# Optimization experiments

Hardware: AMD Instinct MI355X
Metric: run time of the kernel (lower is better)

Reference implementation:

```python
import jax, jax.numpy as jnp
import numpy as np

N, D, R, E = 20000, 256, 12, 200000  # nodes, feat dim, relation labels, edges


def setup_inputs() -> dict:
    key = jax.random.key(0)
    ks = jax.random.split(key, 8)
    x = jax.random.normal(ks[0], (N, D), dtype=jnp.float32)
    dep_idx = jax.random.randint(ks[1], (E,), 0, N)
    rel_idx = jax.random.randint(ks[2], (E,), 0, R)
    gov_idx = jax.random.randint(ks[3], (E,), 0, N)
    # nn.Linear params: W is [out,in], y = x @ W.T + b
    W_self = jax.random.normal(ks[4], (D, D), dtype=jnp.float32) * 0.02
    b_self = jnp.zeros((D,), dtype=jnp.float32)
    # 2R relation weights: [0..R) forward labels, [R..2R) reversed '_r' labels
    W_rel = jax.random.normal(ks[5], (2 * R, D, D), dtype=jnp.float32) * 0.02
    b_rel = jax.random.normal(ks[6], (2 * R, D), dtype=jnp.float32) * 0.02
    return {"x": x, "dep_idx": dep_idx, "rel_idx": rel_idx, "gov_idx": gov_idx,
            "W_self": W_self, "b_self": b_self, "W_rel": W_rel, "b_rel": b_rel}


def reference(x, dep_idx, rel_idx, gov_idx, W_self, b_self, W_rel, b_rel):
    R_ = W_rel.shape[0] // 2
    # self transform for every node
    out = x @ W_self.T + b_self  # [N, D]
    # all-relation transform, grouped GEMM instead of per-edge Linear calls
    T = jnp.einsum('nd,rod->nro', x, W_rel)  # [N, 2R, D]
    # forward edges: dependent += W[rel] @ x[governor] + b[rel]
    msg_f = T[gov_idx, rel_idx] + b_rel[rel_idx]          # [E, D]
    # reverse edges: governor += W[rel_r] @ x[dependent] + b[rel_r]
    msg_r = T[dep_idx, rel_idx + R_] + b_rel[rel_idx + R_]  # [E, D]
    out = out.at[dep_idx].add(msg_f).at[gov_idx].add(msg_r)
    return jax.nn.relu(out)
```

## Files before the change

### kernel.cpp

```cpp
#include <hip/hip_runtime.h>
#include <cstdint>
#include <cstddef>

#define DD 256
#define NSLOT 25
#define SELFSLOT 12

typedef unsigned short u16;
typedef __bf16 bf16t;
typedef bf16t bf16x8 __attribute__((ext_vector_type(8)));
typedef unsigned short us8 __attribute__((ext_vector_type(8)));
typedef unsigned short us4 __attribute__((ext_vector_type(4)));
typedef float f32x4 __attribute__((ext_vector_type(4)));

__device__ __forceinline__ u16 f2bf(float f) {
    uint32_t u = __builtin_bit_cast(uint32_t, f);
    u += 0x7FFFu + ((u >> 16) & 1u);
    return (u16)(u >> 16);
}
__device__ __forceinline__ float bf2f(u16 h) {
    uint32_t u = ((uint32_t)h) << 16;
    return __builtin_bit_cast(float, u);
}

__global__ void k_prep(const float* __restrict__ x, const float* __restrict__ W_rel,
                       const float* __restrict__ W_self, const float* __restrict__ b_self,
                       const float* __restrict__ b_rel,
                       u16* __restrict__ xb, u16* __restrict__ Wb, float* __restrict__ ba,
                       const int* __restrict__ dep, const int* __restrict__ rel,
                       const int* __restrict__ gov, int E, int N, int SG,
                       int* __restrict__ flag, int* __restrict__ bcnt, int NDD) {
    if (blockIdx.x < 1024) {
        const int s0 = NDD;
        const int s1 = s0 + 12 * 65536;
        const int s2 = s1 + 65536;
        const int s3 = s2 + 12 * 65536;
        const int s4 = s3 + NSLOT * DD;
        int i = blockIdx.x * 256 + threadIdx.x;
        int st = 1024 * 256;
        for (; i < s4; i += st) {
            if (i < s0) {
                xb[i] = f2bf(x[i]);
            } else if (i < s1) {
                int k = i - s0; Wb[k] = f2bf(W_rel[k]);
            } else if (i < s2) {
                int k = i - s1; Wb[12 * 65536 + k] = f2bf(W_self[k]);
            } else if (i < s3) {
                int k = i - s2; Wb[13 * 65536 + k] = f2bf(W_rel[12 * 65536 + k]);
            } else {
                int k = i - s3;
                float v;
                if (k < 12 * DD) v = b_rel[k];
                else if (k < 13 * DD) v = b_self[k - 12 * DD];
                else v = b_rel[k - DD];
                ba[k] = v;
            }
        }
    } else {
        int i = (blockIdx.x - 1024) * 256 + threadIdx.x;
        int st = 512 * 256;
        for (int j = i; j < E; j += st) {
            int r = rel[j], d = dep[j], g = gov[j];
            flag[r * N + g] = 1;
            flag[(13 + r) * N + d] = 1;
            atomicAdd(&bcnt[(r / SG) * N + d], 1);
            atomicAdd(&bcnt[((13 + r) / SG) * N + g], 1);
        }
        for (int j = i; j < N; j += st) flag[SELFSLOT * N + j] = 1;
    }
}

__global__ void k_scan1d(const int* __restrict__ A, int* __restrict__ outA,
                         int* __restrict__ bsumA, int lenA, int nbA,
                         const int* __restrict__ B, int* __restrict__ outB,
                         int* __restrict__ bsumB, int lenB) {
    __shared__ int sm[256];
    const int* in; int* outp; int* bs; int len; int lb;
    if ((int)blockIdx.x < nbA) { in = A; outp = outA; bs = bsumA; len = lenA; lb = blockIdx.x; }
    else { in = B; outp = outB; bs = bsumB; len = lenB; lb = blockIdx.x - nbA; }
    int tid = threadIdx.x;
    int i = lb * 256 + tid;
    int v = (i < len) ? in[i] : 0;
    sm[tid] = v;
    __syncthreads();
    for (int off = 1; off < 256; off <<= 1) {
        int t = (tid >= off) ? sm[tid - off] : 0;
        __syncthreads();
        sm[tid] += t;
        __syncthreads();
    }
    if (i < len) outp[i] = sm[tid] - v;
    if (tid == 255) bs[lb] = sm[255];
}

__global__ void k_scan2d(const int* __restrict__ bsumA, int* __restrict__ bbasA, int nbA,
                         const int* __restrict__ bsumB, int* __restrict__ bbasB, int nbB) {
    __shared__ int sm[256];
    int t = threadIdx.x;
    for (int which = 0; which < 2; ++which) {
        const int* bsum = which ? bsumB : bsumA;
        int* bbase = which ? bbasB : bbasA;
        int nb = which ? nbB : nbA;
        int pre[8];
        int tot = 0;
        for (int j = 0; j < 8; ++j) {
            int idx = t * 8 + j;
            int v = (idx < nb) ? bsum[idx] : 0;
            pre[j] = tot;
            tot += v;
        }
        sm[t] = tot;
        __syncthreads();
        for (int off = 1; off < 256; off <<= 1) {
            int x = (t >= off) ? sm[t - off] : 0;
            __syncthreads();
            sm[t] += x;
            __syncthreads();
        }
        int base = sm[t] - tot;
        for (int j = 0; j < 8; ++j) {
            int idx = t * 8 + j;
            if (idx < nb) bbase[idx] = base + pre[j];
        }
        __syncthreads();
    }
}

__global__ void k_scan3d(int* __restrict__ pos, const int* __restrict__ bbasA,
                         const int* __restrict__ flag, int NN, int N,
                         int* __restrict__ rksrc,
                         int* __restrict__ bcsr, int* __restrict__ bcur,
                         const int* __restrict__ bbasB, int B2, int E2) {
    int i = blockIdx.x * 256 + threadIdx.x;
    if (i < NN) {
        int v = pos[i] + bbasA[i >> 8];
        pos[i] = v;
        if (i == NN - 1) pos[NN] = v + flag[i];
        if (flag[i]) {
            int slot = i / N;
            rksrc[v] = i - slot * N;
        }
    }
    if (i < B2) {
        int v = bcsr[i] + bbasB[i >> 8];
        bcsr[i] = v;
        bcur[i] = v;
    }
    if (i == 0) bcsr[B2] = E2;
}

__global__ __launch_bounds__(256, 4) void k_T(
    const u16* __restrict__ xb, const u16* __restrict__ Wb, const float* __restrict__ ba,
    const int* __restrict__ pos, const int* __restrict__ rksrc, u16* __restrict__ T,
    int N, int gslot0, int Sg,
    const int* __restrict__ dep, const int* __restrict__ rel, const int* __restrict__ gov,
    int E, int SG, int* __restrict__ bcur, int* __restrict__ epay, int nScat) {
    __shared__ u16 sm[2 * 128 * 72];
    __shared__ int s_src[128];
    u16 (*As)[72] = (u16(*)[72])sm;
    u16 (*Bs)[72] = (u16(*)[72])(sm + 128 * 72);

    const int tid = threadIdx.x;
    if ((int)blockIdx.x < nScat) {
        int i = blockIdx.x * 256 + tid;
        int st = nScat * 256;
        for (; i < E; i += st) {
            int r = rel[i], d = dep[i], g = gov[i];
            int g0 = r / SG;
            int p = atomicAdd(&bcur[g0 * N + d], 1);
            epay[p] = pos[r * N + g] - pos[g0 * SG * N];
            int gs = 13 + r;
            int g1 = gs / SG;
            int q = atomicAdd(&bcur[g1 * N + g], 1);
            epay[q] = pos[gs * N + d] - pos[g1 * SG * N];
        }
        return;
    }

    const int bx = blockIdx.x - nScat;
    const int mtile = bx / (2 * Sg);
    const int rem = bx - mtile * 2 * Sg;
    const int slot = rem >> 1;
    const int n0 = (rem & 1) * 128;
    const int gslot = gslot0 + slot;
    const int u0 = pos[gslot * N];
    const int used = pos[(gslot + 1) * N] - u0;
    const int row0 = mtile * 128;
    if (row0 >= used) return;
    const int gbase = pos[gslot0 * N];

    if (tid < 128) {
        int r = row0 + tid;
        s_src[tid] = rksrc[u0 + ((r < used) ? r : (used - 1))];
    }
    __syncthreads();

    const int lane = tid & 63, wv = tid >> 6;
    const int wr = wv & 1, wc = wv >> 1;
    const int l15 = lane & 15, quad = lane >> 4;
    const int srow = tid >> 1, sh = (tid & 1) * 32;
    const u16* bgp = Wb + ((size_t)gslot << 16) + (size_t)(n0 + srow) * DD + sh;

    f32x4 acc[4][4] = {};
    for (int kb = 0; kb < DD; kb += 64) {
        {
            const us8* ga = (const us8*)(xb + (size_t)s_src[srow] * DD + kb + sh);
            us8 a0 = ga[0], a1 = ga[1], a2 = ga[2], a3 = ga[3];
            *(us8*)&As[srow][sh]      = a0;
            *(us8*)&As[srow][sh + 8]  = a1;
            *(us8*)&As[srow][sh + 16] = a2;
            *(us8*)&As[srow][sh + 24] = a3;
            const us8* gb = (const us8*)(bgp + kb);
            us8 b0 = gb[0], b1 = gb[1], b2 = gb[2], b3 = gb[3];
            *(us8*)&Bs[srow][sh]      = b0;
            *(us8*)&Bs[srow][sh + 8]  = b1;
            *(us8*)&Bs[srow][sh + 16] = b2;
            *(us8*)&Bs[srow][sh + 24] = b3;
        }
        __syncthreads();
        #pragma unroll
        for (int ks = 0; ks < 2; ++ks) {
            const int kk = ks * 32 + quad * 8;
            bf16x8 af[4], bfv[4];
            #pragma unroll
            for (int mt = 0; mt < 4; ++mt)
                af[mt] = __builtin_bit_cast(bf16x8, *(const us8*)&As[wr * 64 + mt * 16 + l15][kk]);
            #pragma unroll
            for (int nt = 0; nt < 4; ++nt)
                bfv[nt] = __builtin_bit_cast(bf16x8, *(const us8*)&Bs[wc * 64 + nt * 16 + l15][kk]);
            #pragma unroll
            for (int nt = 0; nt < 4; ++nt)
                #pragma unroll
                for (int mt = 0; mt < 4; ++mt)
                    acc[nt][mt] = __builtin_amdgcn_mfma_f32_16x16x32_bf16(
                        bfv[nt], af[mt], acc[nt][mt], 0, 0, 0);
        }
        __syncthreads();
    }

    f32x4 bb[4];
    #pragma unroll
    for (int nt = 0; nt < 4; ++nt)
        bb[nt] = *(const f32x4*)(ba + gslot * DD + n0 + wc * 64 + nt * 16 + quad * 4);
    u16* trb = sm + wv * (64 * 72);
    #pragma unroll
    for (int mt = 0; mt < 4; ++mt)
        #pragma unroll
        for (int nt = 0; nt < 4; ++nt) {
            us4 t4;
            #pragma unroll
            for (int j = 0; j < 4; ++j) t4[j] = f2bf(acc[nt][mt][j] + bb[nt][j]);
            *(us4*)&trb[(size_t)(mt * 16 + l15) * 72 + nt * 16 + quad * 4] = t4;
        }
    __syncthreads();
    const int trow0 = u0 - gbase + row0 + wr * 64;
    const int half = lane & 1;
    #pragma unroll
    for (int it = 0; it < 2; ++it) {
        int r = it * 32 + (lane >> 1);
        if (row0 + wr * 64 + r < used) {
            const us8* sp = (const us8*)(trb + r * 72 + half * 32);
            us8 v0 = sp[0], v1 = sp[1], v2 = sp[2], v3 = sp[3];
            us8* dp = (us8*)(T + (size_t)(trow0 + r) * DD + n0 + wc * 64 + half * 32);
            dp[0] = v0; dp[1] = v1; dp[2] = v2; dp[3] = v3;
        }
    }
}

__global__ __launch_bounds__(256) void k_gather(
    const u16* __restrict__ T, const int* __restrict__ epay,
    const int* __restrict__ csr, const int* __restrict__ pos,
    float* __restrict__ out, int N, int bktBase, int selfKeyBase, int gfN,
    int first, int last) {
    int wid = (blockIdx.x * 256 + threadIdx.x) >> 6;
    if (wid >= N) return;
    int feat = (threadIdx.x & 63) * 4;
    f32x4 a = {0.0f, 0.0f, 0.0f, 0.0f};
    if (!first) a = *(const f32x4*)(out + (size_t)wid * DD + feat);
    if (selfKeyBase >= 0) {
        int p = pos[selfKeyBase + wid] - pos[gfN];
        us4 v = *(const us4*)(T + (size_t)p * DD + feat);
        a[0] += bf2f(v[0]); a[1] += bf2f(v[1]); a[2] += bf2f(v[2]); a[3] += bf2f(v[3]);
    }
    int beg = csr[bktBase + wid], end = csr[bktBase + wid + 1];
    f32x4 b = {0, 0, 0, 0}, c = {0, 0, 0, 0}, d4 = {0, 0, 0, 0};
    int j = beg;
    for (; j + 7 < end; j += 8) {
        int p0 = epay[j],     p1 = epay[j + 1], p2 = epay[j + 2], p3 = epay[j + 3];
        int p4 = epay[j + 4], p5 = epay[j + 5], p6 = epay[j + 6], p7 = epay[j + 7];
        us4 v0 = *(const us4*)(T + (size_t)p0 * DD + feat);
        us4 v1 = *(const us4*)(T + (size_t)p1 * DD + feat);
        us4 v2 = *(const us4*)(T + (size_t)p2 * DD + feat);
        us4 v3 = *(const us4*)(T + (size_t)p3 * DD + feat);
        us4 v4 = *(const us4*)(T + (size_t)p4 * DD + feat);
        us4 v5 = *(const us4*)(T + (size_t)p5 * DD + feat);
        us4 v6 = *(const us4*)(T + (size_t)p6 * DD + feat);
        us4 v7 = *(const us4*)(T + (size_t)p7 * DD + feat);
        #pragma unroll
        for (int t = 0; t < 4; ++t) {
            a[t]  += bf2f(v0[t]) + bf2f(v4[t]);
            b[t]  += bf2f(v1[t]) + bf2f(v5[t]);
            c[t]  += bf2f(v2[t]) + bf2f(v6[t]);
            d4[t] += bf2f(v3[t]) + bf2f(v7[t]);
        }
    }
    for (; j + 1 < end; j += 2) {
        int p0 = epay[j], p1 = epay[j + 1];
        us4 v0 = *(const us4*)(T + (size_t)p0 * DD + feat);
        us4 v1 = *(const us4*)(T + (size_t)p1 * DD + feat);
        #pragma unroll
        for (int t = 0; t < 4; ++t) { a[t] += bf2f(v0[t]); b[t] += bf2f(v1[t]); }
    }
    if (j < end) {
        int p0 = epay[j];
        us4 v0 = *(const us4*)(T + (size_t)p0 * DD + feat);
        #pragma unroll
        for (int t = 0; t < 4; ++t) a[t] += bf2f(v0[t]);
    }
    #pragma unroll
    for (int t = 0; t < 4; ++t) a[t] += b[t] + c[t] + d4[t];
    if (last) {
        #pragma unroll
        for (int t = 0; t < 4; ++t) a[t] = fmaxf(a[t], 0.0f);
    }
    *(f32x4*)(out + (size_t)wid * DD + feat) = a;
}

extern "C" void kernel_launch(void* const* d_in, const int* in_sizes, int n_in,
                              void* d_out, int out_size, void* d_ws, size_t ws_size,
                              hipStream_t stream) {
    const float* x      = (const float*)d_in[0];
    const int*   dep    = (const int*)  d_in[1];
    const int*   rel    = (const int*)  d_in[2];
    const int*   gov    = (const int*)  d_in[3];
    const float* W_self = (const float*)d_in[4];
    const float* b_self = (const float*)d_in[5];
    const float* W_rel  = (const float*)d_in[6];
    const float* b_rel  = (const float*)d_in[7];
    float* out = (float*)d_out;

    const int N  = in_sizes[0] / DD;
    const int E  = in_sizes[1];
    const int NN = NSLOT * N;

    char* w = (char*)d_ws;
    auto alloc = [&](size_t bytes) {
        char* p = w;
        w += (bytes + 255) & ~(size_t)255;
        return p;
    };
    u16* xb    = (u16*)alloc((size_t)N * DD * sizeof(u16));
    u16* Wb    = (u16*)alloc((size_t)NSLOT * DD * DD * sizeof(u16));
    float* ba  = (float*)alloc((size_t)NSLOT * DD * sizeof(float));
    int* flag  = (int*)alloc((size_t)NN * sizeof(int));
    int* pos   = (int*)alloc(((size_t)NN + 1) * sizeof(int));
    int* rksrc = (int*)alloc(((size_t)2 * E + N) * sizeof(int));
    int* bcnt  = (int*)alloc((size_t)6 * N * sizeof(int));
    int* bcsr  = (int*)alloc(((size_t)6 * N + 1) * sizeof(int));
    int* bcur  = (int*)alloc((size_t)6 * N * sizeof(int));
    int* bsumA = (int*)alloc((size_t)2048 * sizeof(int));
    int* bbasA = (int*)alloc((size_t)2048 * sizeof(int));
    int* bsumB = (int*)alloc((size_t)2048 * sizeof(int));
    int* bbasB = (int*)alloc((size_t)2048 * sizeof(int));
    int* epay  = (int*)alloc((size_t)2 * E * sizeof(int));

    size_t used = (size_t)(w - (char*)d_ws);
    size_t avail = (ws_size > used) ? (ws_size - used) : 0;

    int NGROUP = 2, SG = 13;
    for (int ng = 1; ng <= 5; ++ng) {
        int sg = (NSLOT + ng - 1) / ng;
        size_t maxB = 0;
        for (int g = 0; g < ng; ++g) {
            int s0 = g * sg, s1 = s0 + sg; if (s1 > NSLOT) s1 = NSLOT;
            if (s0 >= NSLOT) break;
            int hasSelf = (s0 <= SELFSLOT && SELFSLOT < s1) ? 1 : 0;
            size_t rels = (size_t)(s1 - s0 - hasSelf);
            size_t rows = rels * N; if (rows > (size_t)2 * E) rows = (size_t)2 * E;
            rows += hasSelf ? (size_t)N : 0;
            if (rows > maxB) maxB = rows;
        }
        if (maxB * ((size_t)DD * 2) <= avail) { NGROUP = ng; SG = sg; break; }
        NGROUP = ng + 1; SG = (NSLOT + NGROUP - 1) / NGROUP;
    }
    u16* T = (u16*)w;
    const int B2 = NGROUP * N;

    hipMemsetAsync(flag, 0, (size_t)NN * sizeof(int), stream);
    hipMemsetAsync(bcnt, 0, (size_t)B2 * sizeof(int), stream);
    k_prep<<<1536, 256, 0, stream>>>(x, W_rel, W_self, b_self, b_rel, xb, Wb, ba,
                                     dep, rel, gov, E, N, SG, flag, bcnt, N * DD);

    const int nbA = (NN + 255) / 256;
    const int nbB = (B2 + 255) / 256;
    k_scan1d<<<nbA + nbB, 256, 0, stream>>>(flag, pos, bsumA, NN, nbA, bcnt, bcsr, bsumB, B2);
    k_scan2d<<<1, 256, 0, stream>>>(bsumA, bbasA, nbA, bsumB, bbasB, nbB);
    k_scan3d<<<nbA, 256, 0, stream>>>(pos, bbasA, flag, NN, N, rksrc, bcsr, bcur, bbasB, B2, 2 * E);

    const int tilesPerSlot = (N + 127) / 128;
    const int gBlocks = (N + 3) / 4;
    for (int g = 0; g < NGROUP; ++g) {
        int s0 = g * SG;
        if (s0 >= NSLOT) break;
        int Sg = NSLOT - s0; if (Sg > SG) Sg = SG;
        int nScat = (g == 0) ? 256 : 0;
        k_T<<<dim3(nScat + tilesPerSlot * Sg * 2), 256, 0, stream>>>(
            xb, Wb, ba, pos, rksrc, T, N, s0, Sg,
            dep, rel, gov, E, SG, bcur, epay, nScat);
        int hasSelf = (s0 <= SELFSLOT && SELFSLOT < s0 + Sg);
        k_gather<<<gBlocks, 256, 0, stream>>>(
            T, epay, bcsr, pos, out, N, g * N,
            hasSelf ? SELFSLOT * N : -1, s0 * N,
            (g == 0) ? 1 : 0, (g == NGROUP - 1) ? 1 : 0);
    }
}
```

Baseline: 260.7 us.

## Replace flag prefix scan with atomic per-slot compaction for unique rows

```diff
diff --git a/kernel.cpp b/kernel.cpp
--- a/kernel.cpp
+++ b/kernel.cpp
@@ -29,7 +29,9 @@
                        u16* __restrict__ xb, u16* __restrict__ Wb, float* __restrict__ ba,
                        const int* __restrict__ dep, const int* __restrict__ rel,
                        const int* __restrict__ gov, int E, int N, int SG,
-                       int* __restrict__ flag, int* __restrict__ bcnt, int NDD) {
+                       int* __restrict__ flag, int* __restrict__ slotcnt,
+                       int* __restrict__ bcnt, int* __restrict__ pos,
+                       int* __restrict__ rkpad, int NDD) {
     if (blockIdx.x < 1024) {
         const int s0 = NDD;
         const int s1 = s0 + 12 * 65536;
@@ -57,30 +59,53 @@
             }
         }
     } else {
+        __shared__ int lcnt[NSLOT], lbase[NSLOT];
+        if (threadIdx.x < NSLOT) lcnt[threadIdx.x] = 0;
+        __syncthreads();
         int i = (blockIdx.x - 1024) * 256 + threadIdx.x;
         int st = 512 * 256;
+        int wslot[4], wloc[4], wkey[4], wsrc[4];
+        int nw = 0;
         for (int j = i; j < E; j += st) {
             int r = rel[j], d = dep[j], g = gov[j];
-            flag[r * N + g] = 1;
-            flag[(13 + r) * N + d] = 1;
             atomicAdd(&bcnt[(r / SG) * N + d], 1);
             atomicAdd(&bcnt[((13 + r) / SG) * N + g], 1);
-        }
-        for (int j = i; j < N; j += st) flag[SELFSLOT * N + j] = 1;
-    }
-}
-
-__global__ void k_scan1d(const int* __restrict__ A, int* __restrict__ outA,
-                         int* __restrict__ bsumA, int lenA, int nbA,
-                         const int* __restrict__ B, int* __restrict__ outB,
-                         int* __restrict__ bsumB, int lenB) {
+            int kf = r * N + g;
+            if (atomicCAS(&flag[kf], 0, 1) == 0) {
+                wslot[nw] = r; wkey[nw] = kf; wsrc[nw] = g;
+                wloc[nw] = atomicAdd(&lcnt[r], 1);
+                ++nw;
+            }
+            int sr = 13 + r;
+            int kr = sr * N + d;
+            if (atomicCAS(&flag[kr], 0, 1) == 0) {
+                wslot[nw] = sr; wkey[nw] = kr; wsrc[nw] = d;
+                wloc[nw] = atomicAdd(&lcnt[sr], 1);
+                ++nw;
+            }
+        }
+        for (int j = i; j < N; j += st) {
+            pos[SELFSLOT * N + j] = j;
+            rkpad[SELFSLOT * N + j] = j;
+        }
+        __syncthreads();
+        if (threadIdx.x < NSLOT && lcnt[threadIdx.x] > 0)
+            lbase[threadIdx.x] = atomicAdd(&slotcnt[threadIdx.x], lcnt[threadIdx.x]);
+        __syncthreads();
+        for (int wv = 0; wv < nw; ++wv) {
+            int g = lbase[wslot[wv]] + wloc[wv];
+            pos[wkey[wv]] = g;
+            rkpad[wslot[wv] * N + g] = wsrc[wv];
+        }
+    }
+}
+
+__global__ void k_scan1(const int* __restrict__ B, int* __restrict__ outB,
+                        int* __restrict__ bsumB, int lenB) {
     __shared__ int sm[256];
-    const int* in; int* outp; int* bs; int len; int lb;
-    if ((int)blockIdx.x < nbA) { in = A; outp = outA; bs = bsumA; len = lenA; lb = blockIdx.x; }
-    else { in = B; outp = outB; bs = bsumB; len = lenB; lb = blockIdx.x - nbA; }
     int tid = threadIdx.x;
-    int i = lb * 256 + tid;
-    int v = (i < len) ? in[i] : 0;
+    int i = blockIdx.x * 256 + tid;
+    int v = (i < lenB) ? B[i] : 0;
     sm[tid] = v;
     __syncthreads();
     for (int off = 1; off < 256; off <<= 1) {
@@ -89,58 +114,48 @@
         sm[tid] += t;
         __syncthreads();
     }
-    if (i < len) outp[i] = sm[tid] - v;
-    if (tid == 255) bs[lb] = sm[255];
-}
-
-__global__ void k_scan2d(const int* __restrict__ bsumA, int* __restrict__ bbasA, int nbA,
-                         const int* __restrict__ bsumB, int* __restrict__ bbasB, int nbB) {
+    if (i < lenB) outB[i] = sm[tid] - v;
+    if (tid == 255) bsumB[blockIdx.x] = sm[255];
+}
+
+__global__ void k_scan2(const int* __restrict__ slotcnt, int* __restrict__ slotbase, int N,
+                        const int* __restrict__ bsumB, int* __restrict__ bbasB, int nbB) {
     __shared__ int sm[256];
     int t = threadIdx.x;
-    for (int which = 0; which < 2; ++which) {
-        const int* bsum = which ? bsumB : bsumA;
-        int* bbase = which ? bbasB : bbasA;
-        int nb = which ? nbB : nbA;
-        int pre[8];
-        int tot = 0;
-        for (int j = 0; j < 8; ++j) {
-            int idx = t * 8 + j;
-            int v = (idx < nb) ? bsum[idx] : 0;
-            pre[j] = tot;
-            tot += v;
-        }
-        sm[t] = tot;
-        __syncthreads();
-        for (int off = 1; off < 256; off <<= 1) {
-            int x = (t >= off) ? sm[t - off] : 0;
-            __syncthreads();
-            sm[t] += x;
-            __syncthreads();
-        }
-        int base = sm[t] - tot;
-        for (int j = 0; j < 8; ++j) {
-            int idx = t * 8 + j;
-            if (idx < nb) bbase[idx] = base + pre[j];
-        }
-        __syncthreads();
-    }
-}
-
-__global__ void k_scan3d(int* __restrict__ pos, const int* __restrict__ bbasA,
-                         const int* __restrict__ flag, int NN, int N,
-                         int* __restrict__ rksrc,
-                         int* __restrict__ bcsr, int* __restrict__ bcur,
-                         const int* __restrict__ bbasB, int B2, int E2) {
+    if (t == 0) {
+        int s = 0;
+        for (int k = 0; k < NSLOT; ++k) {
+            slotbase[k] = s;
+            s += (k == SELFSLOT) ? N : slotcnt[k];
+        }
+        slotbase[NSLOT] = s;
+    }
+    int pre[8];
+    int tot = 0;
+    for (int j = 0; j < 8; ++j) {
+        int idx = t * 8 + j;
+        int v = (idx < nbB) ? bsumB[idx] : 0;
+        pre[j] = tot;
+        tot += v;
+    }
+    sm[t] = tot;
+    __syncthreads();
+    for (int off = 1; off < 256; off <<= 1) {
+        int x = (t >= off) ? sm[t - off] : 0;
+        __syncthreads();
+        sm[t] += x;
+        __syncthreads();
+    }
+    int base = sm[t] - tot;
+    for (int j = 0; j < 8; ++j) {
+        int idx = t * 8 + j;
+        if (idx < nbB) bbasB[idx] = base + pre[j];
+    }
+}
+
+__global__ void k_scan3(int* __restrict__ bcsr, int* __restrict__ bcur,
+                        const int* __restrict__ bbasB, int B2, int E2) {
     int i = blockIdx.x * 256 + threadIdx.x;
-    if (i < NN) {
-        int v = pos[i] + bbasA[i >> 8];
-        pos[i] = v;
-        if (i == NN - 1) pos[NN] = v + flag[i];
-        if (flag[i]) {
-            int slot = i / N;
-            rksrc[v] = i - slot * N;
-        }
-    }
     if (i < B2) {
         int v = bcsr[i] + bbasB[i >> 8];
         bcsr[i] = v;
@@ -151,7 +166,8 @@
 
 __global__ __launch_bounds__(256, 4) void k_T(
     const u16* __restrict__ xb, const u16* __restrict__ Wb, const float* __restrict__ ba,
-    const int* __restrict__ pos, const int* __restrict__ rksrc, u16* __restrict__ T,
+    const int* __restrict__ slotbase, const int* __restrict__ pos,
+    const int* __restrict__ rkpad, u16* __restrict__ T,
     int N, int gslot0, int Sg,
     const int* __restrict__ dep, const int* __restrict__ rel, const int* __restrict__ gov,
     int E, int SG, int* __restrict__ bcur, int* __restrict__ epay, int nScat) {
@@ -168,11 +184,11 @@
             int r = rel[i], d = dep[i], g = gov[i];
             int g0 = r / SG;
             int p = atomicAdd(&bcur[g0 * N + d], 1);
-            epay[p] = pos[r * N + g] - pos[g0 * SG * N];
+            epay[p] = slotbase[r] + pos[r * N + g] - slotbase[g0 * SG];
             int gs = 13 + r;
             int g1 = gs / SG;
             int q = atomicAdd(&bcur[g1 * N + g], 1);
-            epay[q] = pos[gs * N + d] - pos[g1 * SG * N];
+            epay[q] = slotbase[gs] + pos[gs * N + d] - slotbase[g1 * SG];
         }
         return;
     }
@@ -183,15 +199,15 @@
     const int slot = rem >> 1;
     const int n0 = (rem & 1) * 128;
     const int gslot = gslot0 + slot;
-    const int u0 = pos[gslot * N];
-    const int used = pos[(gslot + 1) * N] - u0;
+    const int u0 = slotbase[gslot];
+    const int used = slotbase[gslot + 1] - u0;
     const int row0 = mtile * 128;
     if (row0 >= used) return;
-    const int gbase = pos[gslot0 * N];
+    const int gbase = slotbase[gslot0];
 
     if (tid < 128) {
         int r = row0 + tid;
-        s_src[tid] = rksrc[u0 + ((r < used) ? r : (used - 1))];
+        s_src[tid] = rkpad[gslot * N + ((r < used) ? r : (used - 1))];
     }
     __syncthreads();
 
@@ -269,16 +285,16 @@
 
 __global__ __launch_bounds__(256) void k_gather(
     const u16* __restrict__ T, const int* __restrict__ epay,
-    const int* __restrict__ csr, const int* __restrict__ pos,
-    float* __restrict__ out, int N, int bktBase, int selfKeyBase, int gfN,
+    const int* __restrict__ csr, const int* __restrict__ slotbase,
+    float* __restrict__ out, int N, int bktBase, int hasSelf, int s0,
     int first, int last) {
     int wid = (blockIdx.x * 256 + threadIdx.x) >> 6;
     if (wid >= N) return;
     int feat = (threadIdx.x & 63) * 4;
     f32x4 a = {0.0f, 0.0f, 0.0f, 0.0f};
     if (!first) a = *(const f32x4*)(out + (size_t)wid * DD + feat);
-    if (selfKeyBase >= 0) {
-        int p = pos[selfKeyBase + wid] - pos[gfN];
+    if (hasSelf) {
+        int p = slotbase[SELFSLOT] - slotbase[s0] + wid;
         us4 v = *(const us4*)(T + (size_t)p * DD + feat);
         a[0] += bf2f(v[0]); a[1] += bf2f(v[1]); a[2] += bf2f(v[2]); a[3] += bf2f(v[3]);
     }
@@ -352,17 +368,18 @@
     u16* xb    = (u16*)alloc((size_t)N * DD * sizeof(u16));
     u16* Wb    = (u16*)alloc((size_t)NSLOT * DD * DD * sizeof(u16));
     float* ba  = (float*)alloc((size_t)NSLOT * DD * sizeof(float));
-    int* flag  = (int*)alloc((size_t)NN * sizeof(int));
-    int* pos   = (int*)alloc(((size_t)NN + 1) * sizeof(int));
-    int* rksrc = (int*)alloc(((size_t)2 * E + N) * sizeof(int));
-    int* bcnt  = (int*)alloc((size_t)6 * N * sizeof(int));
-    int* bcsr  = (int*)alloc(((size_t)6 * N + 1) * sizeof(int));
-    int* bcur  = (int*)alloc((size_t)6 * N * sizeof(int));
-    int* bsumA = (int*)alloc((size_t)2048 * sizeof(int));
-    int* bbasA = (int*)alloc((size_t)2048 * sizeof(int));
-    int* bsumB = (int*)alloc((size_t)2048 * sizeof(int));
-    int* bbasB = (int*)alloc((size_t)2048 * sizeof(int));
-    int* epay  = (int*)alloc((size_t)2 * E * sizeof(int));
+    int* flag    = (int*)alloc((size_t)NN * sizeof(int));
+    int* slotcnt = (int*)alloc((size_t)32 * sizeof(int));
+    int* bcnt    = (int*)alloc((size_t)6 * N * sizeof(int));
+    char* zend = w;
+    int* pos     = (int*)alloc((size_t)NN * sizeof(int));
+    int* rkpad   = (int*)alloc((size_t)NSLOT * N * sizeof(int));
+    int* slotbase= (int*)alloc((size_t)32 * sizeof(int));
+    int* bcsr    = (int*)alloc(((size_t)6 * N + 1) * sizeof(int));
+    int* bcur    = (int*)alloc((size_t)6 * N * sizeof(int));
+    int* bsumB   = (int*)alloc((size_t)2048 * sizeof(int));
+    int* bbasB   = (int*)alloc((size_t)2048 * sizeof(int));
+    int* epay    = (int*)alloc((size_t)2 * E * sizeof(int));
 
     size_t used = (size_t)(w - (char*)d_ws);
     size_t avail = (ws_size > used) ? (ws_size - used) : 0;
@@ -386,16 +403,15 @@
     u16* T = (u16*)w;
     const int B2 = NGROUP * N;
 
-    hipMemsetAsync(flag, 0, (size_t)NN * sizeof(int), stream);
-    hipMemsetAsync(bcnt, 0, (size_t)B2 * sizeof(int), stream);
+    hipMemsetAsync(flag, 0, (size_t)(zend - (char*)flag), stream);
     k_prep<<<1536, 256, 0, stream>>>(x, W_rel, W_self, b_self, b_rel, xb, Wb, ba,
-                                     dep, rel, gov, E, N, SG, flag, bcnt, N * DD);
-
-    const int nbA = (NN + 255) / 256;
+                                     dep, rel, gov, E, N, SG,
+                                     flag, slotcnt, bcnt, pos, rkpad, N * DD);
+
     const int nbB = (B2 + 255) / 256;
-    k_scan1d<<<nbA + nbB, 256, 0, stream>>>(flag, pos, bsumA, NN, nbA, bcnt, bcsr, bsumB, B2);
-    k_scan2d<<<1, 256, 0, stream>>>(bsumA, bbasA, nbA, bsumB, bbasB, nbB);
-    k_scan3d<<<nbA, 256, 0, stream>>>(pos, bbasA, flag, NN, N, rksrc, bcsr, bcur, bbasB, B2, 2 * E);
+    k_scan1<<<nbB, 256, 0, stream>>>(bcnt, bcsr, bsumB, B2);
+    k_scan2<<<1, 256, 0, stream>>>(slotcnt, slotbase, N, bsumB, bbasB, nbB);
+    k_scan3<<<nbB, 256, 0, stream>>>(bcsr, bcur, bbasB, B2, 2 * E);
 
     const int tilesPerSlot = (N + 127) / 128;
     const int gBlocks = (N + 3) / 4;
@@ -405,12 +421,11 @@
         int Sg = NSLOT - s0; if (Sg > SG) Sg = SG;
         int nScat = (g == 0) ? 256 : 0;
         k_T<<<dim3(nScat + tilesPerSlot * Sg * 2), 256, 0, stream>>>(
-            xb, Wb, ba, pos, rksrc, T, N, s0, Sg,
+            xb, Wb, ba, slotbase, pos, rkpad, T, N, s0, Sg,
             dep, rel, gov, E, SG, bcur, epay, nScat);
-        int hasSelf = (s0 <= SELFSLOT && SELFSLOT < s0 + Sg);
+        int hasSelf = (s0 <= SELFSLOT && SELFSLOT < s0 + Sg) ? 1 : 0;
         k_gather<<<gBlocks, 256, 0, stream>>>(
-            T, epay, bcsr, pos, out, N, g * N,
-            hasSelf ? SELFSLOT * N : -1, s0 * N,
+            T, epay, bcsr, slotbase, out, N, g * N, hasSelf, s0,
             (g == 0) ? 1 : 0, (g == NGROUP - 1) ? 1 : 0);
     }
 }
```

Result: slower. 282.3 us (+8.3%).

## Swizzle GEMM shared-memory tiles, vectorize prep conversion, raise k_T occupancy

Applied to the files above, without the earlier changes.

```diff
diff --git a/kernel.cpp b/kernel.cpp
--- a/kernel.cpp
+++ b/kernel.cpp
@@ -36,25 +36,30 @@
         const int s2 = s1 + 65536;
         const int s3 = s2 + 12 * 65536;
         const int s4 = s3 + NSLOT * DD;
+        const int t4 = s4 >> 2;
         int i = blockIdx.x * 256 + threadIdx.x;
-        int st = 1024 * 256;
-        for (; i < s4; i += st) {
-            if (i < s0) {
-                xb[i] = f2bf(x[i]);
-            } else if (i < s1) {
-                int k = i - s0; Wb[k] = f2bf(W_rel[k]);
-            } else if (i < s2) {
-                int k = i - s1; Wb[12 * 65536 + k] = f2bf(W_self[k]);
-            } else if (i < s3) {
-                int k = i - s2; Wb[13 * 65536 + k] = f2bf(W_rel[12 * 65536 + k]);
-            } else {
-                int k = i - s3;
-                float v;
-                if (k < 12 * DD) v = b_rel[k];
-                else if (k < 13 * DD) v = b_self[k - 12 * DD];
-                else v = b_rel[k - DD];
-                ba[k] = v;
+        const int st = 1024 * 256;
+        for (; i < t4; i += st) {
+            int e = i << 2;
+            const float* src; u16* dst;
+            if (e < s0)      { src = x + e;                    dst = xb + e; }
+            else if (e < s1) { src = W_rel + (e - s0);         dst = Wb + (e - s0); }
+            else if (e < s2) { src = W_self + (e - s1);        dst = Wb + 12 * 65536 + (e - s1); }
+            else if (e < s3) { src = W_rel + 12 * 65536 + (e - s2); dst = Wb + 13 * 65536 + (e - s2); }
+            else {
+                int k = e - s3;
+                const float* bsrc;
+                if (k < 12 * DD) bsrc = b_rel + k;
+                else if (k < 13 * DD) bsrc = b_self + (k - 12 * DD);
+                else bsrc = b_rel + (k - DD);
+                *(f32x4*)(ba + k) = *(const f32x4*)bsrc;
+                continue;
             }
+            f32x4 v = *(const f32x4*)src;
+            us4 o;
+            #pragma unroll
+            for (int j = 0; j < 4; ++j) o[j] = f2bf(v[j]);
+            *(us4*)dst = o;
         }
     } else {
         int i = (blockIdx.x - 1024) * 256 + threadIdx.x;
@@ -149,16 +154,15 @@
     if (i == 0) bcsr[B2] = E2;
 }
 
-__global__ __launch_bounds__(256, 4) void k_T(
+__global__ __launch_bounds__(256, 5) void k_T(
     const u16* __restrict__ xb, const u16* __restrict__ Wb, const float* __restrict__ ba,
     const int* __restrict__ pos, const int* __restrict__ rksrc, u16* __restrict__ T,
     int N, int gslot0, int Sg,
     const int* __restrict__ dep, const int* __restrict__ rel, const int* __restrict__ gov,
     int E, int SG, int* __restrict__ bcur, int* __restrict__ epay, int nScat) {
-    __shared__ u16 sm[2 * 128 * 72];
-    __shared__ int s_src[128];
-    u16 (*As)[72] = (u16(*)[72])sm;
-    u16 (*Bs)[72] = (u16(*)[72])(sm + 128 * 72);
+    __shared__ u16 sm[2 * 128 * 64];
+    u16* As = sm;
+    u16* Bs = sm + 128 * 64;
 
     const int tid = threadIdx.x;
     if ((int)blockIdx.x < nScat) {
@@ -189,45 +193,56 @@
     if (row0 >= used) return;
     const int gbase = pos[gslot0 * N];
 
-    if (tid < 128) {
-        int r = row0 + tid;
-        s_src[tid] = rksrc[u0 + ((r < used) ? r : (used - 1))];
-    }
-    __syncthreads();
-
     const int lane = tid & 63, wv = tid >> 6;
     const int wr = wv & 1, wc = wv >> 1;
     const int l15 = lane & 15, quad = lane >> 4;
     const int srow = tid >> 1, sh = (tid & 1) * 32;
+
+    int arow = row0 + srow;
+    if (arow >= used) arow = used - 1;
+    const int asrc = rksrc[u0 + arow];
+    const u16* agp = xb + (size_t)asrc * DD + sh;
     const u16* bgp = Wb + ((size_t)gslot << 16) + (size_t)(n0 + srow) * DD + sh;
+
+    const int sc0 = sh >> 3;
+    const int sx = srow & 7;
+    int so[4];
+    #pragma unroll
+    for (int c = 0; c < 4; ++c) so[c] = srow * 64 + (((sc0 + c) ^ sx) << 3);
 
     f32x4 acc[4][4] = {};
     for (int kb = 0; kb < DD; kb += 64) {
         {
-            const us8* ga = (const us8*)(xb + (size_t)s_src[srow] * DD + kb + sh);
+            const us8* ga = (const us8*)(agp + kb);
             us8 a0 = ga[0], a1 = ga[1], a2 = ga[2], a3 = ga[3];
-            *(us8*)&As[srow][sh]      = a0;
-            *(us8*)&As[srow][sh + 8]  = a1;
-            *(us8*)&As[srow][sh + 16] = a2;
-            *(us8*)&As[srow][sh + 24] = a3;
+            *(us8*)&As[so[0]] = a0;
+            *(us8*)&As[so[1]] = a1;
+            *(us8*)&As[so[2]] = a2;
+            *(us8*)&As[so[3]] = a3;
             const us8* gb = (const us8*)(bgp + kb);
             us8 b0 = gb[0], b1 = gb[1], b2 = gb[2], b3 = gb[3];
-            *(us8*)&Bs[srow][sh]      = b0;
-            *(us8*)&Bs[srow][sh + 8]  = b1;
-            *(us8*)&Bs[srow][sh + 16] = b2;
-            *(us8*)&Bs[srow][sh + 24] = b3;
+            *(us8*)&Bs[so[0]] = b0;
+            *(us8*)&Bs[so[1]] = b1;
+            *(us8*)&Bs[so[2]] = b2;
+            *(us8*)&Bs[so[3]] = b3;
         }
         __syncthreads();
         #pragma unroll
         for (int ks = 0; ks < 2; ++ks) {
-            const int kk = ks * 32 + quad * 8;
+            const int ck = ks * 4 + quad;
             bf16x8 af[4], bfv[4];
             #pragma unroll
-            for (int mt = 0; mt < 4; ++mt)
-                af[mt] = __builtin_bit_cast(bf16x8, *(const us8*)&As[wr * 64 + mt * 16 + l15][kk]);
+            for (int mt = 0; mt < 4; ++mt) {
+                int r = wr * 64 + mt * 16 + l15;
+                af[mt] = __builtin_bit_cast(bf16x8,
+                    *(const us8*)&As[r * 64 + ((ck ^ (r & 7)) << 3)]);
+            }
             #pragma unroll
-            for (int nt = 0; nt < 4; ++nt)
-                bfv[nt] = __builtin_bit_cast(bf16x8, *(const us8*)&Bs[wc * 64 + nt * 16 + l15][kk]);
+            for (int nt = 0; nt < 4; ++nt) {
+                int r = wc * 64 + nt * 16 + l15;
+                bfv[nt] = __builtin_bit_cast(bf16x8,
+                    *(const us8*)&Bs[r * 64 + ((ck ^ (r & 7)) << 3)]);
+            }
             #pragma unroll
             for (int nt = 0; nt < 4; ++nt)
                 #pragma unroll
@@ -242,16 +257,20 @@
     #pragma unroll
     for (int nt = 0; nt < 4; ++nt)
         bb[nt] = *(const f32x4*)(ba + gslot * DD + n0 + wc * 64 + nt * 16 + quad * 4);
-    u16* trb = sm + wv * (64 * 72);
+    u16* trb = sm + wv * 4096;
     #pragma unroll
-    for (int mt = 0; mt < 4; ++mt)
+    for (int mt = 0; mt < 4; ++mt) {
+        int m = mt * 16 + l15;
+        int mx = m & 7;
         #pragma unroll
         for (int nt = 0; nt < 4; ++nt) {
             us4 t4;
             #pragma unroll
             for (int j = 0; j < 4; ++j) t4[j] = f2bf(acc[nt][mt][j] + bb[nt][j]);
-            *(us4*)&trb[(size_t)(mt * 16 + l15) * 72 + nt * 16 + quad * 4] = t4;
-        }
+            int col = nt * 16 + quad * 4;
+            *(us4*)&trb[m * 64 + (((col >> 3) ^ mx) << 3) + (col & 7)] = t4;
+        }
+    }
     __syncthreads();
     const int trow0 = u0 - gbase + row0 + wr * 64;
     const int half = lane & 1;
@@ -259,8 +278,11 @@
     for (int it = 0; it < 2; ++it) {
         int r = it * 32 + (lane >> 1);
         if (row0 + wr * 64 + r < used) {
-            const us8* sp = (const us8*)(trb + r * 72 + half * 32);
-            us8 v0 = sp[0], v1 = sp[1], v2 = sp[2], v3 = sp[3];
+            int rx = r & 7;
+            us8 v0 = *(const us8*)&trb[r * 64 + (((half * 4 + 0) ^ rx) << 3)];
+            us8 v1 = *(const us8*)&trb[r * 64 + (((half * 4 + 1) ^ rx) << 3)];
+            us8 v2 = *(const us8*)&trb[r * 64 + (((half * 4 + 2) ^ rx) << 3)];
+            us8 v3 = *(const us8*)&trb[r * 64 + (((half * 4 + 3) ^ rx) << 3)];
             us8* dp = (us8*)(T + (size_t)(trow0 + r) * DD + n0 + wc * 64 + half * 32);
             dp[0] = v0; dp[1] = v1; dp[2] = v2; dp[3] = v3;
         }
```

After: 308.4 us. 18.3% more time.
